# Kernel optimization log

Measured on AMD Instinct MI355X. Metric: run time of the kernel, lower is better.

Reference implementation:

```python
import jax, jax.numpy as jnp
import numpy as np

FIELD_DIMS = [100000, 1000, 100, 50]
NUM_FEATURES = 12
NUM_CAT = len(FIELD_DIMS)
NUM_CONT = NUM_FEATURES - NUM_CAT
D = 32            # embed_dim
HID = [64, 32]
B, T = 1024, 200
BN_EPS = 1e-5


def setup_inputs() -> dict:
    key = jax.random.key(0)
    ks = jax.random.split(key, 32)
    # x: [B, T, F]; first NUM_CAT cols are integer category ids stored as float
    cat_cols = [jax.random.randint(ks[i], (B, T, 1), 0, FIELD_DIMS[i]).astype(jnp.float32)
                for i in range(NUM_CAT)]
    cont_cols = jax.random.normal(ks[4], (B, T, NUM_CONT), dtype=jnp.float32)
    x = jnp.concatenate(cat_cols + [cont_cols], axis=-1)
    s = 0.05
    inp = {"x": x}
    for i, fd in enumerate(FIELD_DIMS):
        inp[f"emb{i}"] = jax.random.normal(ks[5 + i], (fd, D), dtype=jnp.float32) * s
        inp[f"lin{i}"] = jax.random.normal(ks[9 + i], (fd, D), dtype=jnp.float32) * s
    # Conv1d(1, D, 1) per continuous field == per-field affine map scalar -> D
    inp["cont_w"]  = jax.random.normal(ks[13], (NUM_CONT, D), dtype=jnp.float32) * s
    inp["cont_b"]  = jax.random.normal(ks[14], (NUM_CONT, D), dtype=jnp.float32) * s
    inp["clin_w"]  = jax.random.normal(ks[15], (NUM_CONT, D), dtype=jnp.float32) * s
    inp["clin_b"]  = jax.random.normal(ks[16], (NUM_CONT, D), dtype=jnp.float32) * s
    inp["fin_bias"] = jnp.zeros((D,), dtype=jnp.float32)
    # DNN tower: kernel_size-1 Conv1d == dense over channel dim
    dims = [NUM_FEATURES * D] + HID
    for li in range(len(HID)):
        fan_in = dims[li]
        inp[f"w{li+1}"] = jax.random.normal(ks[17 + 4 * li], (HID[li], fan_in), dtype=jnp.float32) / np.sqrt(fan_in)
        inp[f"b{li+1}"] = jnp.zeros((HID[li],), dtype=jnp.float32)
        inp[f"g{li+1}"] = jnp.ones((HID[li],), dtype=jnp.float32)
        inp[f"beta{li+1}"] = jnp.zeros((HID[li],), dtype=jnp.float32)
    inp["w_out"] = jax.random.normal(ks[30], (D, HID[-1]), dtype=jnp.float32) / np.sqrt(HID[-1])
    inp["b_out"] = jnp.zeros((D,), dtype=jnp.float32)
    return inp


def _batchnorm(h, g, b):
    # training-mode BN over (batch, time), biased variance (torch default)
    mu = h.mean(axis=(0, 1))
    var = h.var(axis=(0, 1))
    return g * (h - mu) * jax.lax.rsqrt(var + BN_EPS) + b


def reference(x, emb0, emb1, emb2, emb3, lin0, lin1, lin2, lin3,
              cont_w, cont_b, clin_w, clin_b, fin_bias,
              w1, b1, g1, beta1, w2, b2, g2, beta2, w_out, b_out):
    embs = [emb0, emb1, emb2, emb3]
    lins = [lin0, lin1, lin2, lin3]
    cat_idx = x[..., :NUM_CAT].astype(jnp.int32)          # [B,T,C]
    xc = x[..., NUM_CAT:]                                  # [B,T,Nc]

    # per-field embeddings -> [B,T,F,D]
    cat_emb = jnp.stack([embs[i][cat_idx[..., i]] for i in range(NUM_CAT)], axis=2)
    cont_emb = xc[..., None] * cont_w + cont_b             # [B,T,Nc,D]
    emb_all = jnp.concatenate([cat_emb, cont_emb], axis=2)  # [B,T,F,D]

    # FM pairwise interaction (sum-of-squares trick)
    s = emb_all.sum(axis=2)                                # [B,T,D]
    interaction = 0.5 * (s * s - (emb_all * emb_all).sum(axis=2))

    # linear terms
    lin_cat = sum(lins[i][cat_idx[..., i]] for i in range(NUM_CAT))      # [B,T,D]
    lin_cont = (xc[..., None] * clin_w + clin_b).sum(axis=2)             # [B,T,D]
    linear = lin_cat + lin_cont + fin_bias

    # DNN tower (k=1 convs == dense over F*D channels); dropout omitted (eval)
    h = emb_all.reshape(B, T, NUM_FEATURES * D)
    h = jax.nn.relu(_batchnorm(h @ w1.T + b1, g1, beta1))
    h = jax.nn.relu(_batchnorm(h @ w2.T + b2, g2, beta2))
    dnn = h @ w_out.T + b_out                              # [B,T,D]

    return linear + interaction + dnn                      # [B,T,D]
```

## Files before the change

### kernel.cpp

```cpp
#include <hip/hip_runtime.h>
#include <hip/hip_bf16.h>

typedef __hip_bfloat16 bf16;

#define ROWS 204800
#define N_INV (1.0f / 204800.0f)

__device__ float g_stats[256];
__device__ float g_E1_1[1000 * 64];
__device__ float g_E1_2[100 * 64];
__device__ float g_E1_3[50 * 64];
__device__ float g_U[8 * 64];
__device__ float g_Vb[64];
__device__ bf16  g_h1p[ROWS * 64];
__device__ bf16  g_h2p[ROWS * 32];
__device__ bf16  g_fmp[ROWS * 32];

__device__ __forceinline__ int clampi(int v, int hi) {
    return v < 0 ? 0 : (v > hi ? hi : v);
}
__device__ __forceinline__ float rl_f(float v, int l) {
    return __uint_as_float((unsigned int)__builtin_amdgcn_readlane((int)__float_as_uint(v), l));
}

__device__ __forceinline__ int swz8(int d) {
    return (d & ~7) | ((d & 7) ^ ((d >> 3) & 7));
}
__device__ __forceinline__ int swz4(int d) {
    return (d & ~3) | ((d & 3) ^ (((d >> 2) ^ (d >> 4)) & 3));
}

#define GLOAD16(gp, lp)                                                        \
    __builtin_amdgcn_global_load_lds(                                          \
        (const __attribute__((address_space(1))) unsigned int*)(gp),           \
        (__attribute__((address_space(3))) unsigned int*)(lp), 16, 0, 0)

__global__ __launch_bounds__(64) void precompute_kernel(
    const float* __restrict__ emb1, const float* __restrict__ emb2, const float* __restrict__ emb3,
    const float* __restrict__ cont_w, const float* __restrict__ cont_b,
    const float* __restrict__ w1, const float* __restrict__ b1)
{
    int b = blockIdx.x;
    int k = threadIdx.x;
    __shared__ float row[32];

    if (b < 1150) {
        const float* tab; float* out; int i, colOff;
        if (b < 1000)      { tab = emb1; out = g_E1_1; i = b;        colOff = 32; }
        else if (b < 1100) { tab = emb2; out = g_E1_2; i = b - 1000; colOff = 64; }
        else               { tab = emb3; out = g_E1_3; i = b - 1100; colOff = 96; }
        if (k < 32) row[k] = tab[i * 32 + k];
        __syncthreads();
        const float* wr = w1 + k * 384 + colOff;
        float acc = 0.f;
        #pragma unroll
        for (int d = 0; d < 32; ++d) acc = fmaf(row[d], wr[d], acc);
        out[i * 64 + k] = acc;
    } else {
        g_stats[k]       = 0.f;
        g_stats[k + 64]  = 0.f;
        g_stats[k + 128] = 0.f;
        g_stats[k + 192] = 0.f;

        float vb = b1[k];
        #pragma unroll
        for (int j = 0; j < 8; ++j) {
            const float* wr = w1 + k * 384 + (4 + j) * 32;
            float u = 0.f;
            #pragma unroll
            for (int d = 0; d < 32; ++d) {
                float w = wr[d];
                u  = fmaf(cont_w[j * 32 + d], w, u);
                vb = fmaf(cont_b[j * 32 + d], w, vb);
            }
            g_U[j * 64 + k] = u;
        }
        g_Vb[k] = vb;
    }
}

__global__ __launch_bounds__(256, 4) void phase1_kernel(
    const float* __restrict__ x,
    const float* __restrict__ emb0, const float* __restrict__ lin0,
    const float* __restrict__ emb1, const float* __restrict__ lin1,
    const float* __restrict__ emb2, const float* __restrict__ lin2,
    const float* __restrict__ emb3, const float* __restrict__ lin3,
    const float* __restrict__ cont_w, const float* __restrict__ cont_b,
    const float* __restrict__ clin_w, const float* __restrict__ clin_b,
    const float* __restrict__ fin_bias,
    const float* __restrict__ w1)
{
    __shared__ float lsum[64], lsq[64];

    int tid  = threadIdx.x;
    int lane = tid & 63;
    int wv   = tid >> 6;
    int d    = lane & 31;
    bool lo  = lane < 32;

    if (tid < 64) { lsum[tid] = 0.f; lsq[tid] = 0.f; }
    __syncthreads();

    float w1c[32];
    {
        const float4* wrv = (const float4*)(w1 + lane * 384);
        #pragma unroll
        for (int q = 0; q < 8; ++q) {
            float4 v = wrv[q];
            w1c[4*q+0] = v.x; w1c[4*q+1] = v.y;
            w1c[4*q+2] = v.z; w1c[4*q+3] = v.w;
        }
    }

    float uk[8];
    #pragma unroll
    for (int j = 0; j < 8; ++j) uk[j] = g_U[j * 64 + lane];
    float vbk = g_Vb[lane];

    float p1[8], p2[8], fb = 0.f;
    if (lo) {
        #pragma unroll
        for (int j = 0; j < 8; ++j) { p1[j] = cont_w[j * 32 + d]; p2[j] = cont_b[j * 32 + d]; }
    } else {
        #pragma unroll
        for (int j = 0; j < 8; ++j) { p1[j] = clin_w[j * 32 + d]; p2[j] = clin_b[j * 32 + d]; }
        fb = fin_bias[d];
    }

    const float* T0 = lo ? emb0 : lin0;
    const float* T1 = lo ? emb1 : lin1;
    const float* T2 = lo ? emb2 : lin2;
    const float* T3 = lo ? emb3 : lin3;

    int gw   = blockIdx.x * 4 + wv;
    int base = gw * 16;

    float xs[4];
    #pragma unroll
    for (int g = 0; g < 4; ++g)
        xs[g] = (lane < 48) ? x[(base + 4 * g) * 12 + lane] : 0.f;

    float ss = 0.f, qq = 0.f;

    #pragma unroll
    for (int g = 0; g < 4; ++g) {
        float ga[4], gb[4], gc[4], gd[4], t1[4], t2[4], t3[4];
        #pragma unroll
        for (int t = 0; t < 4; ++t) {
            int f  = t * 12;
            int i0 = clampi((int)rl_f(xs[g], f + 0), 99999);
            int i1 = clampi((int)rl_f(xs[g], f + 1), 999);
            int i2 = clampi((int)rl_f(xs[g], f + 2), 99);
            int i3 = clampi((int)rl_f(xs[g], f + 3), 49);
            ga[t] = T0[i0 * 32 + d];
            gb[t] = T1[i1 * 32 + d];
            gc[t] = T2[i2 * 32 + d];
            gd[t] = T3[i3 * 32 + d];
            t1[t] = g_E1_1[i1 * 64 + lane];
            t2[t] = g_E1_2[i2 * 64 + lane];
            t3[t] = g_E1_3[i3 * 64 + lane];
        }

        #pragma unroll
        for (int t = 0; t < 4; ++t) {
            int r  = base + 4 * g + t;
            int fo = t * 12 + 4;
            float xc[8];
            #pragma unroll
            for (int j = 0; j < 8; ++j) xc[j] = rl_f(xs[g], fo + j);

            float va = ga[t], vb = gb[t], vc = gc[t], vd = gd[t];

            float e0a = 0.f, e0b = 0.f, e0c = 0.f, e0d = 0.f;
            #pragma unroll
            for (int dd = 0; dd < 32; dd += 4) {
                e0a = fmaf(rl_f(va, dd + 0), w1c[dd + 0], e0a);
                e0b = fmaf(rl_f(va, dd + 1), w1c[dd + 1], e0b);
                e0c = fmaf(rl_f(va, dd + 2), w1c[dd + 2], e0c);
                e0d = fmaf(rl_f(va, dd + 3), w1c[dd + 3], e0d);
            }
            float e0f = (e0a + e0b) + (e0c + e0d);

            float half_val;
            if (lo) {
                float s0 = va + vb, s1 = vc + vd;
                float q0 = fmaf(va, va, vb * vb);
                float q1 = fmaf(vc, vc, vd * vd);
                #pragma unroll
                for (int j = 0; j < 8; ++j) {
                    float ce = fmaf(xc[j], p1[j], p2[j]);
                    if (j & 1) { s1 += ce; q1 = fmaf(ce, ce, q1); }
                    else       { s0 += ce; q0 = fmaf(ce, ce, q0); }
                }
                float sfull = s0 + s1;
                half_val = 0.5f * (sfull * sfull - (q0 + q1));
            } else {
                float l0 = va + vb + fb, l1 = vc + vd;
                #pragma unroll
                for (int j = 0; j < 8; ++j) {
                    if (j & 1) l1 = fmaf(xc[j], p1[j], l1 + p2[j]);
                    else       l0 = fmaf(xc[j], p1[j], l0 + p2[j]);
                }
                half_val = l0 + l1;
            }
            float other = __shfl(half_val, lane | 32);
            if (lo) g_fmp[r * 32 + d] = __float2bfloat16(half_val + other);

            float h1 = ((vbk + e0f) + (t1[t] + t2[t])) + t3[t];
            #pragma unroll
            for (int j = 0; j < 8; ++j) h1 = fmaf(xc[j], uk[j], h1);

            g_h1p[r * 64 + lane] = __float2bfloat16(h1);
            ss += h1;
            qq = fmaf(h1, h1, qq);
        }
    }

    atomicAdd(&lsum[lane], ss);
    atomicAdd(&lsq[lane], qq);
    __syncthreads();
    if (tid < 64) {
        atomicAdd(&g_stats[tid], lsum[tid]);
        atomicAdd(&g_stats[64 + tid], lsq[tid]);
    }
}

__global__ __launch_bounds__(256) void phase2_kernel(
    const float* __restrict__ w2, const float* __restrict__ b2,
    const float* __restrict__ g1, const float* __restrict__ beta1)
{
    __shared__ float sa[64], sc[64];
    __shared__ float ls[64];
    __shared__ uint4 hbuf[4][512];

    int tid  = threadIdx.x;
    int lane = tid & 63;
    int wv   = tid >> 6;
    size_t rowBase = (size_t)(blockIdx.x * 4 + wv) * 64;

    {
        const char* gsrc = (const char*)g_h1p + rowBase * 128;
        #pragma unroll
        for (int i = 0; i < 8; ++i) {
            int dlin = (i << 6) + lane;
            GLOAD16(gsrc + swz8(dlin) * 16, &hbuf[wv][i << 6]);
        }
    }

    if (tid < 64) {
        float mu  = g_stats[tid] * N_INV;
        float var = g_stats[64 + tid] * N_INV - mu * mu;
        float a   = g1[tid] * rsqrtf(var + 1e-5f);
        sa[tid] = a;
        sc[tid] = beta1[tid] - a * mu;
        ls[tid] = 0.f;
    }
    __syncthreads();
    asm volatile("s_waitcnt vmcnt(0)" ::: "memory");

    const uint4* lrow = hbuf[wv] + (lane << 3);
    int r7 = lane & 7;

    float acc[32];
    #pragma unroll
    for (int m = 0; m < 32; ++m) acc[m] = 0.f;

    #pragma unroll
    for (int half = 0; half < 2; ++half) {
        uint4 u[4];
        #pragma unroll
        for (int q = 0; q < 4; ++q) u[q] = lrow[(half * 4 + q) ^ r7];

        float y[32];
        #pragma unroll
        for (int q = 0; q < 4; ++q) {
            unsigned int w4[4] = {u[q].x, u[q].y, u[q].z, u[q].w};
            #pragma unroll
            for (int j = 0; j < 4; ++j) {
                int i  = q * 4 + j;
                int ch = half * 32 + 2 * i;
                float f0 = __uint_as_float(w4[j] << 16);
                float f1 = __uint_as_float(w4[j] & 0xffff0000u);
                y[2*i]     = fmaxf(0.f, fmaf(sa[ch],     f0, sc[ch]));
                y[2*i + 1] = fmaxf(0.f, fmaf(sa[ch + 1], f1, sc[ch + 1]));
            }
        }

        #pragma unroll
        for (int m = 0; m < 32; ++m) {
            const float* wr = w2 + m * 64 + half * 32;
            float a0 = 0.f, a1 = 0.f, a2 = 0.f, a3 = 0.f;
            #pragma unroll
            for (int k = 0; k < 32; k += 4) {
                a0 = fmaf(y[k + 0], wr[k + 0], a0);
                a1 = fmaf(y[k + 1], wr[k + 1], a1);
                a2 = fmaf(y[k + 2], wr[k + 2], a2);
                a3 = fmaf(y[k + 3], wr[k + 3], a3);
            }
            acc[m] += (a0 + a1) + (a2 + a3);
        }
    }

    #pragma unroll
    for (int m = 0; m < 32; ++m) acc[m] += b2[m];

    uint4 o[4];
    unsigned int* ow = (unsigned int*)o;
    #pragma unroll
    for (int i = 0; i < 16; ++i) {
        unsigned int lo16 = (unsigned int)__bfloat16_as_ushort(__float2bfloat16(acc[2*i]));
        unsigned int hi16 = (unsigned int)__bfloat16_as_ushort(__float2bfloat16(acc[2*i + 1]));
        ow[i] = lo16 | (hi16 << 16);
    }

    #pragma unroll
    for (int q = 0; q < 4; ++q) hbuf[wv][swz4((lane << 2) + q)] = o[q];
    asm volatile("s_waitcnt lgkmcnt(0)" ::: "memory");
    {
        uint4* og = (uint4*)(g_h2p + rowBase * 32);
        #pragma unroll
        for (int i = 0; i < 4; ++i) {
            int dlin = (i << 6) + lane;
            og[dlin] = hbuf[wv][swz4(dlin)];
        }
    }

    #pragma unroll
    for (int c0 = 0; c0 < 32; c0 += 8) {
        float s[8], q[8];
        #pragma unroll
        for (int j = 0; j < 8; ++j) { s[j] = acc[c0 + j]; q[j] = s[j] * s[j]; }
        #pragma unroll
        for (int off = 32; off >= 1; off >>= 1) {
            #pragma unroll
            for (int j = 0; j < 8; ++j) {
                s[j] += __shfl_xor(s[j], off);
                q[j] += __shfl_xor(q[j], off);
            }
        }
        if (lane == 0) {
            #pragma unroll
            for (int j = 0; j < 8; ++j) {
                atomicAdd(&ls[c0 + j],      s[j]);
                atomicAdd(&ls[32 + c0 + j], q[j]);
            }
        }
    }
    __syncthreads();
    if (tid < 32)       atomicAdd(&g_stats[128 + tid], ls[tid]);
    else if (tid < 64)  atomicAdd(&g_stats[160 + (tid - 32)], ls[tid]);
}

__global__ __launch_bounds__(256) void phase3_kernel(
    const float* __restrict__ w_out, const float* __restrict__ b_out,
    const float* __restrict__ g2, const float* __restrict__ beta2,
    float* __restrict__ out)
{
    __shared__ float sa[32], sc[32];
    __shared__ uint4 sbuf[4][512];

    int tid  = threadIdx.x;
    int lane = tid & 63;
    int wv   = tid >> 6;
    size_t rowBase = (size_t)(blockIdx.x * 4 + wv) * 64;

    {
        const char* gh2 = (const char*)g_h2p + rowBase * 64;
        const char* gfm = (const char*)g_fmp + rowBase * 64;
        #pragma unroll
        for (int i = 0; i < 4; ++i) {
            int dlin = (i << 6) + lane;
            GLOAD16(gh2 + swz4(dlin) * 16, &sbuf[wv][i << 6]);
        }
        #pragma unroll
        for (int i = 0; i < 4; ++i) {
            int dlin = (i << 6) + lane;
            GLOAD16(gfm + swz4(dlin) * 16, &sbuf[wv][256 + (i << 6)]);
        }
    }

    if (tid < 32) {
        float mu  = g_stats[128 + tid] * N_INV;
        float var = g_stats[160 + tid] * N_INV - mu * mu;
        float a   = g2[tid] * rsqrtf(var + 1e-5f);
        sa[tid] = a;
        sc[tid] = beta2[tid] - a * mu;
    }
    __syncthreads();
    asm volatile("s_waitcnt vmcnt(0)" ::: "memory");

    uint4 u[4], fm4[4];
    #pragma unroll
    for (int q = 0; q < 4; ++q) {
        int gidx = swz4((lane << 2) + q);
        u[q]   = sbuf[wv][gidx];
        fm4[q] = sbuf[wv][256 + gidx];
    }

    float y2[32];
    #pragma unroll
    for (int q = 0; q < 4; ++q) {
        unsigned int w4[4] = {u[q].x, u[q].y, u[q].z, u[q].w};
        #pragma unroll
        for (int j = 0; j < 4; ++j) {
            int i = q * 4 + j;
            float f0 = __uint_as_float(w4[j] << 16);
            float f1 = __uint_as_float(w4[j] & 0xffff0000u);
            y2[2*i]     = fmaxf(0.f, fmaf(sa[2*i],     f0, sc[2*i]));
            y2[2*i + 1] = fmaxf(0.f, fmaf(sa[2*i + 1], f1, sc[2*i + 1]));
        }
    }

    float fmv[32];
    {
        const unsigned int* fw = (const unsigned int*)fm4;
        #pragma unroll
        for (int i = 0; i < 16; ++i) {
            fmv[2*i]     = __uint_as_float(fw[i] << 16);
            fmv[2*i + 1] = __uint_as_float(fw[i] & 0xffff0000u);
        }
    }

    float res[32];
    #pragma unroll
    for (int dd = 0; dd < 32; ++dd) {
        const float* wr = w_out + dd * 32;
        float a0 = fmv[dd] + b_out[dd], a1 = 0.f, a2 = 0.f, a3 = 0.f;
        #pragma unroll
        for (int k = 0; k < 32; k += 4) {
            a0 = fmaf(y2[k + 0], wr[k + 0], a0);
            a1 = fmaf(y2[k + 1], wr[k + 1], a1);
            a2 = fmaf(y2[k + 2], wr[k + 2], a2);
            a3 = fmaf(y2[k + 3], wr[k + 3], a3);
        }
        res[dd] = (a0 + a1) + (a2 + a3);
    }

    #pragma unroll
    for (int q = 0; q < 8; ++q) {
        uint4 v;
        v.x = __float_as_uint(res[4*q+0]);
        v.y = __float_as_uint(res[4*q+1]);
        v.z = __float_as_uint(res[4*q+2]);
        v.w = __float_as_uint(res[4*q+3]);
        sbuf[wv][swz8((lane << 3) + q)] = v;
    }
    asm volatile("s_waitcnt lgkmcnt(0)" ::: "memory");
    {
        uint4* og = (uint4*)(out + rowBase * 32);
        #pragma unroll
        for (int i = 0; i < 8; ++i) {
            int dlin = (i << 6) + lane;
            og[dlin] = sbuf[wv][swz8(dlin)];
        }
    }
}

extern "C" void kernel_launch(void* const* d_in, const int* in_sizes, int n_in,
                              void* d_out, int out_size, void* d_ws, size_t ws_size,
                              hipStream_t stream) {
    (void)in_sizes; (void)n_in; (void)out_size; (void)d_ws; (void)ws_size;

    const float* x       = (const float*)d_in[0];
    const float* emb0    = (const float*)d_in[1];
    const float* lin0    = (const float*)d_in[2];
    const float* emb1    = (const float*)d_in[3];
    const float* lin1    = (const float*)d_in[4];
    const float* emb2    = (const float*)d_in[5];
    const float* lin2    = (const float*)d_in[6];
    const float* emb3    = (const float*)d_in[7];
    const float* lin3    = (const float*)d_in[8];
    const float* cont_w  = (const float*)d_in[9];
    const float* cont_b  = (const float*)d_in[10];
    const float* clin_w  = (const float*)d_in[11];
    const float* clin_b  = (const float*)d_in[12];
    const float* fin_bias= (const float*)d_in[13];
    const float* w1      = (const float*)d_in[14];
    const float* b1      = (const float*)d_in[15];
    const float* g1      = (const float*)d_in[16];
    const float* beta1   = (const float*)d_in[17];
    const float* w2      = (const float*)d_in[18];
    const float* b2      = (const float*)d_in[19];
    const float* g2      = (const float*)d_in[20];
    const float* beta2   = (const float*)d_in[21];
    const float* w_out   = (const float*)d_in[22];
    const float* b_out   = (const float*)d_in[23];

    float* outp = (float*)d_out;

    hipLaunchKernelGGL(precompute_kernel, dim3(1151), dim3(64), 0, stream,
                       emb1, emb2, emb3, cont_w, cont_b, w1, b1);

    hipLaunchKernelGGL(phase1_kernel, dim3(3200), dim3(256), 0, stream,
                       x, emb0, lin0, emb1, lin1, emb2, lin2, emb3, lin3,
                       cont_w, cont_b, clin_w, clin_b, fin_bias, w1);

    hipLaunchKernelGGL(phase2_kernel, dim3(800), dim3(256), 0, stream,
                       w2, b2, g1, beta1);

    hipLaunchKernelGGL(phase3_kernel, dim3(800), dim3(256), 0, stream,
                       w_out, b_out, g2, beta2, outp);
}
```

Before: 335.2 us.

## Prefetch large-table embedding gathers into LDS and pipeline per-group compute

In phase1, the random gathers from the 100k-row table are issued up front for all four row groups using asynchronous global-to-LDS loads. The remaining small-table gathers are issued one group at a time, with explicit vmcnt waits before each group's compute. The aim is to hide the latency of the cache-missing big-table gathers behind other loads and compute. In exchange it adds 16KB of LDS per block. It also depends on hand-counted vmcnt values, which may over-wait or interact poorly with the compiler's own wait insertion.

```diff
diff --git a/kernel.cpp b/kernel.cpp
--- a/kernel.cpp
+++ b/kernel.cpp
@@ -34,6 +34,16 @@
     __builtin_amdgcn_global_load_lds(                                          \
         (const __attribute__((address_space(1))) unsigned int*)(gp),           \
         (__attribute__((address_space(3))) unsigned int*)(lp), 16, 0, 0)
+#define GLOAD4(gp, lp)                                                         \
+    __builtin_amdgcn_global_load_lds(                                          \
+        (const __attribute__((address_space(1))) unsigned int*)(gp),           \
+        (__attribute__((address_space(3))) unsigned int*)(lp), 4, 0, 0)
+
+#define VWAIT(n)                                                               \
+    do {                                                                       \
+        asm volatile("s_waitcnt vmcnt(" #n ")" ::: "memory");                  \
+        __builtin_amdgcn_sched_barrier(0);                                     \
+    } while (0)
 
 __global__ __launch_bounds__(64) void precompute_kernel(
     const float* __restrict__ emb1, const float* __restrict__ emb2, const float* __restrict__ emb3,
@@ -91,6 +101,7 @@
     const float* __restrict__ w1)
 {
     __shared__ float lsum[64], lsq[64];
+    __shared__ float s_va[4][4][256];
 
     int tid  = threadIdx.x;
     int lane = tid & 63;
@@ -140,19 +151,22 @@
     for (int g = 0; g < 4; ++g)
         xs[g] = (lane < 48) ? x[(base + 4 * g) * 12 + lane] : 0.f;
 
-    float ss = 0.f, qq = 0.f;
-
-    #pragma unroll
-    for (int g = 0; g < 4; ++g) {
-        float ga[4], gb[4], gc[4], gd[4], t1[4], t2[4], t3[4];
+    auto issueL = [&](int g) {
+        #pragma unroll
+        for (int t = 0; t < 4; ++t) {
+            int i0 = clampi((int)rl_f(xs[g], t * 12), 99999);
+            GLOAD4(T0 + i0 * 32 + d, &s_va[wv][g][t * 64]);
+        }
+    };
+
+    float gb[4], gc[4], gd[4], t1[4], t2[4], t3[4];
+    auto issueC = [&](int g) {
         #pragma unroll
         for (int t = 0; t < 4; ++t) {
             int f  = t * 12;
-            int i0 = clampi((int)rl_f(xs[g], f + 0), 99999);
             int i1 = clampi((int)rl_f(xs[g], f + 1), 999);
             int i2 = clampi((int)rl_f(xs[g], f + 2), 99);
             int i3 = clampi((int)rl_f(xs[g], f + 3), 49);
-            ga[t] = T0[i0 * 32 + d];
             gb[t] = T1[i1 * 32 + d];
             gc[t] = T2[i2 * 32 + d];
             gd[t] = T3[i3 * 32 + d];
@@ -160,7 +174,11 @@
             t2[t] = g_E1_2[i2 * 64 + lane];
             t3[t] = g_E1_3[i3 * 64 + lane];
         }
-
+    };
+
+    float ss = 0.f, qq = 0.f;
+
+    auto compute = [&](int g) {
         #pragma unroll
         for (int t = 0; t < 4; ++t) {
             int r  = base + 4 * g + t;
@@ -169,7 +187,8 @@
             #pragma unroll
             for (int j = 0; j < 8; ++j) xc[j] = rl_f(xs[g], fo + j);
 
-            float va = ga[t], vb = gb[t], vc = gc[t], vd = gd[t];
+            float va = s_va[wv][g][t * 64 + lane];
+            float vb = gb[t], vc = gc[t], vd = gd[t];
 
             float e0a = 0.f, e0b = 0.f, e0c = 0.f, e0d = 0.f;
             #pragma unroll
@@ -214,7 +233,14 @@
             ss += h1;
             qq = fmaf(h1, h1, qq);
         }
-    }
+    };
+
+    issueL(0); issueL(1); issueL(2); issueL(3);
+
+    issueC(0); VWAIT(12); compute(0);
+    issueC(1); VWAIT(8);  compute(1);
+    issueC(2); VWAIT(4);  compute(2);
+    issueC(3); VWAIT(0);  compute(3);
 
     atomicAdd(&lsum[lane], ss);
     atomicAdd(&lsq[lane], qq);
```

Result: slower. 346.0 us (+3.2%).
